# Performance work log

Hardware: AMD Instinct MI355X
Metric: run time of the kernel (lower is better)

The kernel has to match this reference:

```python
import jax, jax.numpy as jnp
import numpy as np

H = 128
B = 512
T = 1024
FUT = 64


def setup_inputs() -> dict:
    key = jax.random.key(0)
    ks = jax.random.split(key, 11)
    k = 1.0 / np.sqrt(H)  # torch LSTMCell/Linear init range
    u = lambda kk, shape: jax.random.uniform(kk, shape, jnp.float32, -k, k)
    return {
        "x": jax.random.normal(ks[0], (B, T), jnp.float32),
        "W_ih1": u(ks[1], (4 * H, 1)),
        "b_ih1": u(ks[2], (4 * H,)),
        "W_hh1": u(ks[3], (4 * H, H)),
        "b_hh1": u(ks[4], (4 * H,)),
        "W_ih2": u(ks[5], (4 * H, H)),
        "b_ih2": u(ks[6], (4 * H,)),
        "W_hh2": u(ks[7], (4 * H, H)),
        "b_hh2": u(ks[8], (4 * H,)),
        "W_out": u(ks[9], (1, H)),
        "b_out": u(ks[10], (1,)),
        "future": FUT,
    }


def _cell(x_t, h, c, W_ih, b_ih, W_hh, b_hh):
    # torch.nn.LSTMCell: gates ordered i, f, g, o
    g = x_t @ W_ih.T + h @ W_hh.T + (b_ih + b_hh)
    i, f, gg, o = jnp.split(g, 4, axis=-1)
    c_new = jax.nn.sigmoid(f) * c + jax.nn.sigmoid(i) * jnp.tanh(gg)
    h_new = jax.nn.sigmoid(o) * jnp.tanh(c_new)
    return h_new, c_new


def reference(x, W_ih1, b_ih1, W_hh1, b_hh1, W_ih2, b_ih2, W_hh2, b_hh2, W_out, b_out, future):
    Bn = x.shape[0]
    Hn = W_hh1.shape[1]
    z = jnp.zeros((Bn, Hn), x.dtype)

    def enc_step(carry, x_t):
        h1, c1, h2, c2 = carry
        h1, c1 = _cell(x_t, h1, c1, W_ih1, b_ih1, W_hh1, b_hh1)
        h2, c2 = _cell(h1, h2, c2, W_ih2, b_ih2, W_hh2, b_hh2)
        return (h1, c1, h2, c2), None

    xs = x.T[:, :, None]  # [T, B, 1]
    (h1, c1, h2, c2), _ = jax.lax.scan(enc_step, (z, z, z, z), xs)
    out0 = h2 @ W_out.T + b_out  # [B, 1]

    def fut_step(carry, _):
        h1, c1, h2, c2, out = carry
        h1, c1 = _cell(out, h1, c1, W_ih1, b_ih1, W_hh1, b_hh1)
        h2, c2 = _cell(h1, h2, c2, W_ih2, b_ih2, W_hh2, b_hh2)
        out = h2 @ W_out.T + b_out
        return (h1, c1, h2, c2, out), out

    _, fouts = jax.lax.scan(fut_step, (h1, c1, h2, c2, out0), None, length=future - 1)
    # torch cats [B,1] tensors on dim=1 -> [B, future]
    return jnp.concatenate([out0, fouts[:, :, 0].T], axis=1)
```

## Files before the change

### kernel.cpp

```cpp
#include <hip/hip_runtime.h>

#define HH 128
#define TT 1024
#define NFUT 64
#define MB 2
#define NBLK 256
#define NITER (TT + NFUT)

typedef _Float16 half8 __attribute__((ext_vector_type(8)));
typedef float floatx4 __attribute__((ext_vector_type(4)));

#define MFMA16(a, b, c) __builtin_amdgcn_mfma_f32_16x16x32_f16((a), (b), (c), 0, 0, 0)

__device__ __forceinline__ float sigm(float v) {
  return __builtin_amdgcn_rcpf(1.0f + __builtin_amdgcn_exp2f(v * -1.442695040888963f));
}
__device__ __forceinline__ float tanh_f(float v) {
  float a = __builtin_fabsf(v);
  float e = __builtin_amdgcn_exp2f(a * -2.885390081777927f);
  float r = (1.0f - e) * __builtin_amdgcn_rcpf(1.0f + e);
  return __builtin_copysignf(r, v);
}
__device__ __forceinline__ half8 ldw8(const float* __restrict__ p) {
  half8 r;
#pragma unroll
  for (int i = 0; i < 8; ++i) r[i] = (_Float16)p[i];
  return r;
}

__global__
__attribute__((amdgpu_flat_work_group_size(512, 512), amdgpu_waves_per_eu(2, 2)))
void lstm_kernel(
    const float* __restrict__ x,
    const float* __restrict__ W_ih1, const float* __restrict__ b_ih1,
    const float* __restrict__ W_hh1, const float* __restrict__ b_hh1,
    const float* __restrict__ W_ih2, const float* __restrict__ b_ih2,
    const float* __restrict__ W_hh2, const float* __restrict__ b_hh2,
    const float* __restrict__ W_out, const float* __restrict__ b_out,
    float* __restrict__ out)
{
  __shared__ __align__(16) _Float16 h1b[2][2048];
  __shared__ __align__(16) _Float16 h2b[2][2048];
  __shared__ float xs[TT * MB];
  __shared__ float opart[8 * MB];

  const int tid = (int)threadIdx.x;
  const int lane = tid & 63;
  const int w = tid >> 6;
  const int jl = lane & 15;
  const int rg = lane >> 4;
  const int j = w * 16 + jl;
  const int b0g = (int)blockIdx.x * MB;

  for (int idx = tid; idx < TT * MB; idx += 512) {
    int t = idx & (TT - 1);
    int bb = idx >> 10;
    xs[t * MB + bb] = x[(b0g + bb) * TT + t];
  }
  for (int idx = tid; idx < 2 * 2048; idx += 512) {
    h1b[idx >> 11][idx & 2047] = (_Float16)0.0f;
    h2b[idx >> 11][idx & 2047] = (_Float16)0.0f;
  }

  half8 A00, A01, A02, A03, A10, A11, A12, A13, A20, A21, A22, A23, A30, A31, A32, A33;
  half8 H00, H01, H02, H03, H10, H11, H12, H13, H20, H21, H22, H23, H30, H31, H32, H33;
  half8 I00, I01, I02, I03, I10, I11, I12, I13, I20, I21, I22, I23, I30, I31, I32, I33;
#define LDW(N, Q, P) do { \
    const float* _p = (P) + ((Q) * HH + j) * HH + rg * 8; \
    N##0 = ldw8(_p);      N##1 = ldw8(_p + 32); \
    N##2 = ldw8(_p + 64); N##3 = ldw8(_p + 96); } while (0)
  LDW(A0, 0, W_hh1); LDW(A1, 1, W_hh1); LDW(A2, 2, W_hh1); LDW(A3, 3, W_hh1);
  LDW(H0, 0, W_hh2); LDW(H1, 1, W_hh2); LDW(H2, 2, W_hh2); LDW(H3, 3, W_hh2);
  LDW(I0, 0, W_ih2); LDW(I1, 1, W_ih2); LDW(I2, 2, W_ih2); LDW(I3, 3, W_ih2);

  float bias1[4], bias2[4], wi1[4];
#pragma unroll
  for (int q = 0; q < 4; ++q) {
    bias1[q] = b_ih1[q * HH + j] + b_hh1[q * HH + j];
    bias2[q] = b_ih2[q * HH + j] + b_hh2[q * HH + j];
    wi1[q] = W_ih1[q * HH + j];
  }
  const float wo = W_out[j];
  const float bo = b_out[0];
  float c1a = 0.f, c1b = 0.f, c2a = 0.f, c2b = 0.f;

  __syncthreads();

  const int aoff = lane * 8;
  const int wb = ((j >> 5) << 9) + (((j >> 3) & 3) << 7) + (j & 7);

#define G2K(KF) do { \
    half8 bv = *(const half8*)(&h2b[prv][KF * 512 + aoff]); \
    g0 = MFMA16(bv, H0##KF, g0); g1 = MFMA16(bv, H1##KF, g1); \
    g2 = MFMA16(bv, H2##KF, g2); g3 = MFMA16(bv, H3##KF, g3); \
    half8 aw = *(const half8*)(&h1b[prv][KF * 512 + aoff]); \
    g0 = MFMA16(aw, I0##KF, g0); g1 = MFMA16(aw, I1##KF, g1); \
    g2 = MFMA16(aw, I2##KF, g2); g3 = MFMA16(aw, I3##KF, g3); } while (0)
#define G1K(KF) do { \
    half8 av = *(const half8*)(&h1b[prv][KF * 512 + aoff]); \
    a0 = MFMA16(av, A0##KF, a0); a1 = MFMA16(av, A1##KF, a1); \
    a2 = MFMA16(av, A2##KF, a2); a3 = MFMA16(av, A3##KF, a3); } while (0)

  for (int k = 0; k < NITER; ++k) {
    const int cur = k & 1;
    const int prv = cur ^ 1;

    floatx4 g0 = {0.f,0.f,0.f,0.f}, g1 = {0.f,0.f,0.f,0.f};
    floatx4 g2 = {0.f,0.f,0.f,0.f}, g3 = {0.f,0.f,0.f,0.f};
    __builtin_amdgcn_s_setprio(1);
    G2K(0); G2K(1); G2K(2); G2K(3);
    __builtin_amdgcn_s_setprio(0);

    if (k >= 1) {
      float gi0 = g0[0] + bias2[0], gi1 = g0[1] + bias2[0];
      float gf0 = g1[0] + bias2[1], gf1 = g1[1] + bias2[1];
      float gg0 = g2[0] + bias2[2], gg1 = g2[1] + bias2[2];
      float go0 = g3[0] + bias2[3], go1 = g3[1] + bias2[3];
      c2a = sigm(gf0) * c2a + sigm(gi0) * tanh_f(gg0);
      c2b = sigm(gf1) * c2b + sigm(gi1) * tanh_f(gg1);
      float h20 = sigm(go0) * tanh_f(c2a);
      float h21 = sigm(go1) * tanh_f(c2b);
      if (lane < 16) {
        h2b[cur][wb] = (_Float16)h20;
        h2b[cur][wb + 8] = (_Float16)h21;
      }
      if (k >= TT) {
        float p0 = h20 * wo, p1 = h21 * wo;
        p0 += __shfl_xor(p0, 1); p1 += __shfl_xor(p1, 1);
        p0 += __shfl_xor(p0, 2); p1 += __shfl_xor(p1, 2);
        p0 += __shfl_xor(p0, 4); p1 += __shfl_xor(p1, 4);
        p0 += __shfl_xor(p0, 8); p1 += __shfl_xor(p1, 8);
        if (lane == 0) {
          opart[w * MB + 0] = p0;
          opart[w * MB + 1] = p1;
        }
      }
    }

    floatx4 a0 = {0.f,0.f,0.f,0.f}, a1 = {0.f,0.f,0.f,0.f};
    floatx4 a2 = {0.f,0.f,0.f,0.f}, a3 = {0.f,0.f,0.f,0.f};
    __builtin_amdgcn_s_setprio(1);
    G1K(0); G1K(1); G1K(2); G1K(3);
    __builtin_amdgcn_s_setprio(0);

    float x0, x1;
    if (k < TT) {
      x0 = xs[k * MB + 0];
      x1 = xs[k * MB + 1];
    } else {
      __syncthreads();
      float s0 = bo, s1 = bo;
#pragma unroll
      for (int p = 0; p < 8; ++p) {
        s0 += opart[p * MB + 0];
        s1 += opart[p * MB + 1];
      }
      x0 = s0; x1 = s1;
      if (w == 0 && lane < MB) out[(b0g + lane) * NFUT + (k - TT)] = (lane == 0) ? s0 : s1;
    }

    if (k <= NITER - 2) {
      float gi0 = a0[0] + x0 * wi1[0] + bias1[0], gi1 = a0[1] + x1 * wi1[0] + bias1[0];
      float gf0 = a1[0] + x0 * wi1[1] + bias1[1], gf1 = a1[1] + x1 * wi1[1] + bias1[1];
      float gg0 = a2[0] + x0 * wi1[2] + bias1[2], gg1 = a2[1] + x1 * wi1[2] + bias1[2];
      float go0 = a3[0] + x0 * wi1[3] + bias1[3], go1 = a3[1] + x1 * wi1[3] + bias1[3];
      c1a = sigm(gf0) * c1a + sigm(gi0) * tanh_f(gg0);
      c1b = sigm(gf1) * c1b + sigm(gi1) * tanh_f(gg1);
      float h10 = sigm(go0) * tanh_f(c1a);
      float h11 = sigm(go1) * tanh_f(c1b);
      if (lane < 16) {
        h1b[cur][wb] = (_Float16)h10;
        h1b[cur][wb + 8] = (_Float16)h11;
      }
    }
    __syncthreads();
    __builtin_amdgcn_sched_barrier(0);
  }
}

extern "C" void kernel_launch(void* const* d_in, const int* in_sizes, int n_in,
                              void* d_out, int out_size, void* d_ws, size_t ws_size,
                              hipStream_t stream) {
  const float* x     = (const float*)d_in[0];
  const float* W_ih1 = (const float*)d_in[1];
  const float* b_ih1 = (const float*)d_in[2];
  const float* W_hh1 = (const float*)d_in[3];
  const float* b_hh1 = (const float*)d_in[4];
  const float* W_ih2 = (const float*)d_in[5];
  const float* b_ih2 = (const float*)d_in[6];
  const float* W_hh2 = (const float*)d_in[7];
  const float* b_hh2 = (const float*)d_in[8];
  const float* W_out = (const float*)d_in[9];
  const float* b_out = (const float*)d_in[10];
  (void)in_sizes; (void)n_in; (void)out_size; (void)d_ws; (void)ws_size;

  lstm_kernel<<<dim3(NBLK), dim3(512), 0, stream>>>(
      x, W_ih1, b_ih1, W_hh1, b_hh1, W_ih2, b_ih2, W_hh2, b_hh2, W_out, b_out,
      (float*)d_out);
}
```

Before: 1.582 ms.

## Halve block to 4 waves, each computing two 16-row hidden slices per gate

```diff
diff --git a/kernel.cpp b/kernel.cpp
--- a/kernel.cpp
+++ b/kernel.cpp
@@ -29,7 +29,7 @@
 }
 
 __global__
-__attribute__((amdgpu_flat_work_group_size(512, 512), amdgpu_waves_per_eu(2, 2)))
+__attribute__((amdgpu_flat_work_group_size(256, 256), amdgpu_waves_per_eu(1, 1)))
 void lstm_kernel(
     const float* __restrict__ x,
     const float* __restrict__ W_ih1, const float* __restrict__ b_ih1,
@@ -42,116 +42,148 @@
   __shared__ __align__(16) _Float16 h1b[2][2048];
   __shared__ __align__(16) _Float16 h2b[2][2048];
   __shared__ float xs[TT * MB];
-  __shared__ float opart[8 * MB];
+  __shared__ float opart[4 * MB];
 
   const int tid = (int)threadIdx.x;
   const int lane = tid & 63;
   const int w = tid >> 6;
   const int jl = lane & 15;
   const int rg = lane >> 4;
-  const int j = w * 16 + jl;
   const int b0g = (int)blockIdx.x * MB;
 
-  for (int idx = tid; idx < TT * MB; idx += 512) {
+  for (int idx = tid; idx < TT * MB; idx += 256) {
     int t = idx & (TT - 1);
     int bb = idx >> 10;
     xs[t * MB + bb] = x[(b0g + bb) * TT + t];
   }
-  for (int idx = tid; idx < 2 * 2048; idx += 512) {
+  for (int idx = tid; idx < 2 * 2048; idx += 256) {
     h1b[idx >> 11][idx & 2047] = (_Float16)0.0f;
     h2b[idx >> 11][idx & 2047] = (_Float16)0.0f;
   }
 
-  half8 A00, A01, A02, A03, A10, A11, A12, A13, A20, A21, A22, A23, A30, A31, A32, A33;
-  half8 H00, H01, H02, H03, H10, H11, H12, H13, H20, H21, H22, H23, H30, H31, H32, H33;
-  half8 I00, I01, I02, I03, I10, I11, I12, I13, I20, I21, I22, I23, I30, I31, I32, I33;
-#define LDW(N, Q, P) do { \
-    const float* _p = (P) + ((Q) * HH + j) * HH + rg * 8; \
-    N##0 = ldw8(_p);      N##1 = ldw8(_p + 32); \
-    N##2 = ldw8(_p + 64); N##3 = ldw8(_p + 96); } while (0)
-  LDW(A0, 0, W_hh1); LDW(A1, 1, W_hh1); LDW(A2, 2, W_hh1); LDW(A3, 3, W_hh1);
-  LDW(H0, 0, W_hh2); LDW(H1, 1, W_hh2); LDW(H2, 2, W_hh2); LDW(H3, 3, W_hh2);
-  LDW(I0, 0, W_ih2); LDW(I1, 1, W_ih2); LDW(I2, 2, W_ih2); LDW(I3, 3, W_ih2);
-
-  float bias1[4], bias2[4], wi1[4];
+  half8 A00,A01,A02,A03, A10,A11,A12,A13, A20,A21,A22,A23, A30,A31,A32,A33,
+        A40,A41,A42,A43, A50,A51,A52,A53, A60,A61,A62,A63, A70,A71,A72,A73;
+  half8 H00,H01,H02,H03, H10,H11,H12,H13, H20,H21,H22,H23, H30,H31,H32,H33,
+        H40,H41,H42,H43, H50,H51,H52,H53, H60,H61,H62,H63, H70,H71,H72,H73;
+  half8 I00,I01,I02,I03, I10,I11,I12,I13, I20,I21,I22,I23, I30,I31,I32,I33,
+        I40,I41,I42,I43, I50,I51,I52,I53, I60,I61,I62,I63, I70,I71,I72,I73;
+#define LDWS(N, S, Q, T, P) do { \
+    const float* _p = (P) + ((Q) * HH + (w * 32 + (T) * 16 + jl)) * HH + rg * 8; \
+    N##S##0 = ldw8(_p);      N##S##1 = ldw8(_p + 32); \
+    N##S##2 = ldw8(_p + 64); N##S##3 = ldw8(_p + 96); } while (0)
+  LDWS(A,0,0,0,W_hh1); LDWS(A,1,0,1,W_hh1); LDWS(A,2,1,0,W_hh1); LDWS(A,3,1,1,W_hh1);
+  LDWS(A,4,2,0,W_hh1); LDWS(A,5,2,1,W_hh1); LDWS(A,6,3,0,W_hh1); LDWS(A,7,3,1,W_hh1);
+  LDWS(H,0,0,0,W_hh2); LDWS(H,1,0,1,W_hh2); LDWS(H,2,1,0,W_hh2); LDWS(H,3,1,1,W_hh2);
+  LDWS(H,4,2,0,W_hh2); LDWS(H,5,2,1,W_hh2); LDWS(H,6,3,0,W_hh2); LDWS(H,7,3,1,W_hh2);
+  LDWS(I,0,0,0,W_ih2); LDWS(I,1,0,1,W_ih2); LDWS(I,2,1,0,W_ih2); LDWS(I,3,1,1,W_ih2);
+  LDWS(I,4,2,0,W_ih2); LDWS(I,5,2,1,W_ih2); LDWS(I,6,3,0,W_ih2); LDWS(I,7,3,1,W_ih2);
+
+  float b1[8], b2[8], w1[8];
 #pragma unroll
   for (int q = 0; q < 4; ++q) {
-    bias1[q] = b_ih1[q * HH + j] + b_hh1[q * HH + j];
-    bias2[q] = b_ih2[q * HH + j] + b_hh2[q * HH + j];
-    wi1[q] = W_ih1[q * HH + j];
-  }
-  const float wo = W_out[j];
+#pragma unroll
+    for (int t = 0; t < 2; ++t) {
+      int s = q * 2 + t;
+      int jt = w * 32 + t * 16 + jl;
+      b1[s] = b_ih1[q * HH + jt] + b_hh1[q * HH + jt];
+      b2[s] = b_ih2[q * HH + jt] + b_hh2[q * HH + jt];
+      w1[s] = W_ih1[q * HH + jt];
+    }
+  }
+  const float wo0 = W_out[w * 32 + jl];
+  const float wo1 = W_out[w * 32 + 16 + jl];
   const float bo = b_out[0];
-  float c1a = 0.f, c1b = 0.f, c2a = 0.f, c2b = 0.f;
+  float c1_00 = 0.f, c1_01 = 0.f, c1_10 = 0.f, c1_11 = 0.f;
+  float c2_00 = 0.f, c2_01 = 0.f, c2_10 = 0.f, c2_11 = 0.f;
 
   __syncthreads();
 
   const int aoff = lane * 8;
-  const int wb = ((j >> 5) << 9) + (((j >> 3) & 3) << 7) + (j & 7);
-
-#define G2K(KF) do { \
-    half8 bv = *(const half8*)(&h2b[prv][KF * 512 + aoff]); \
-    g0 = MFMA16(bv, H0##KF, g0); g1 = MFMA16(bv, H1##KF, g1); \
-    g2 = MFMA16(bv, H2##KF, g2); g3 = MFMA16(bv, H3##KF, g3); \
-    half8 aw = *(const half8*)(&h1b[prv][KF * 512 + aoff]); \
-    g0 = MFMA16(aw, I0##KF, g0); g1 = MFMA16(aw, I1##KF, g1); \
-    g2 = MFMA16(aw, I2##KF, g2); g3 = MFMA16(aw, I3##KF, g3); } while (0)
-#define G1K(KF) do { \
-    half8 av = *(const half8*)(&h1b[prv][KF * 512 + aoff]); \
-    a0 = MFMA16(av, A0##KF, a0); a1 = MFMA16(av, A1##KF, a1); \
-    a2 = MFMA16(av, A2##KF, a2); a3 = MFMA16(av, A3##KF, a3); } while (0)
+  const int j0 = w * 32 + jl, j1 = j0 + 16;
+  const int wb0 = ((j0 >> 5) << 9) + (((j0 >> 3) & 3) << 7) + (j0 & 7);
+  const int wb1 = ((j1 >> 5) << 9) + (((j1 >> 3) & 3) << 7) + (j1 & 7);
+
+#define C2K(K) do { \
+    half8 bv = *(const half8*)(&h2b[prv][K * 512 + aoff]); \
+    p0 = MFMA16(bv, H0##K, p0); p1 = MFMA16(bv, H1##K, p1); \
+    p2 = MFMA16(bv, H2##K, p2); p3 = MFMA16(bv, H3##K, p3); \
+    p4 = MFMA16(bv, H4##K, p4); p5 = MFMA16(bv, H5##K, p5); \
+    p6 = MFMA16(bv, H6##K, p6); p7 = MFMA16(bv, H7##K, p7); \
+    half8 aw = *(const half8*)(&h1b[prv][K * 512 + aoff]); \
+    p0 = MFMA16(aw, I0##K, p0); p1 = MFMA16(aw, I1##K, p1); \
+    p2 = MFMA16(aw, I2##K, p2); p3 = MFMA16(aw, I3##K, p3); \
+    p4 = MFMA16(aw, I4##K, p4); p5 = MFMA16(aw, I5##K, p5); \
+    p6 = MFMA16(aw, I6##K, p6); p7 = MFMA16(aw, I7##K, p7); } while (0)
+#define C1K(K) do { \
+    half8 av = *(const half8*)(&h1b[prv][K * 512 + aoff]); \
+    p0 = MFMA16(av, A0##K, p0); p1 = MFMA16(av, A1##K, p1); \
+    p2 = MFMA16(av, A2##K, p2); p3 = MFMA16(av, A3##K, p3); \
+    p4 = MFMA16(av, A4##K, p4); p5 = MFMA16(av, A5##K, p5); \
+    p6 = MFMA16(av, A6##K, p6); p7 = MFMA16(av, A7##K, p7); } while (0)
 
   for (int k = 0; k < NITER; ++k) {
     const int cur = k & 1;
     const int prv = cur ^ 1;
-
-    floatx4 g0 = {0.f,0.f,0.f,0.f}, g1 = {0.f,0.f,0.f,0.f};
-    floatx4 g2 = {0.f,0.f,0.f,0.f}, g3 = {0.f,0.f,0.f,0.f};
-    __builtin_amdgcn_s_setprio(1);
-    G2K(0); G2K(1); G2K(2); G2K(3);
-    __builtin_amdgcn_s_setprio(0);
+    const bool fut = (k >= TT);
+    const bool doC1 = (k <= NITER - 2);
+
+    floatx4 p0 = {0.f,0.f,0.f,0.f}, p1 = {0.f,0.f,0.f,0.f};
+    floatx4 p2 = {0.f,0.f,0.f,0.f}, p3 = {0.f,0.f,0.f,0.f};
+    floatx4 p4 = {0.f,0.f,0.f,0.f}, p5 = {0.f,0.f,0.f,0.f};
+    floatx4 p6 = {0.f,0.f,0.f,0.f}, p7 = {0.f,0.f,0.f,0.f};
+    C2K(0); C2K(1); C2K(2); C2K(3);
 
     if (k >= 1) {
-      float gi0 = g0[0] + bias2[0], gi1 = g0[1] + bias2[0];
-      float gf0 = g1[0] + bias2[1], gf1 = g1[1] + bias2[1];
-      float gg0 = g2[0] + bias2[2], gg1 = g2[1] + bias2[2];
-      float go0 = g3[0] + bias2[3], go1 = g3[1] + bias2[3];
-      c2a = sigm(gf0) * c2a + sigm(gi0) * tanh_f(gg0);
-      c2b = sigm(gf1) * c2b + sigm(gi1) * tanh_f(gg1);
-      float h20 = sigm(go0) * tanh_f(c2a);
-      float h21 = sigm(go1) * tanh_f(c2b);
+      float h2_00, h2_01, h2_10, h2_11;
+      {
+        float gi = p0[0] + b2[0], gf = p2[0] + b2[2], gg = p4[0] + b2[4], go = p6[0] + b2[6];
+        c2_00 = sigm(gf) * c2_00 + sigm(gi) * tanh_f(gg);
+        h2_00 = sigm(go) * tanh_f(c2_00);
+        gi = p0[1] + b2[0]; gf = p2[1] + b2[2]; gg = p4[1] + b2[4]; go = p6[1] + b2[6];
+        c2_01 = sigm(gf) * c2_01 + sigm(gi) * tanh_f(gg);
+        h2_01 = sigm(go) * tanh_f(c2_01);
+        gi = p1[0] + b2[1]; gf = p3[0] + b2[3]; gg = p5[0] + b2[5]; go = p7[0] + b2[7];
+        c2_10 = sigm(gf) * c2_10 + sigm(gi) * tanh_f(gg);
+        h2_10 = sigm(go) * tanh_f(c2_10);
+        gi = p1[1] + b2[1]; gf = p3[1] + b2[3]; gg = p5[1] + b2[5]; go = p7[1] + b2[7];
+        c2_11 = sigm(gf) * c2_11 + sigm(gi) * tanh_f(gg);
+        h2_11 = sigm(go) * tanh_f(c2_11);
+      }
       if (lane < 16) {
-        h2b[cur][wb] = (_Float16)h20;
-        h2b[cur][wb + 8] = (_Float16)h21;
-      }
-      if (k >= TT) {
-        float p0 = h20 * wo, p1 = h21 * wo;
-        p0 += __shfl_xor(p0, 1); p1 += __shfl_xor(p1, 1);
-        p0 += __shfl_xor(p0, 2); p1 += __shfl_xor(p1, 2);
-        p0 += __shfl_xor(p0, 4); p1 += __shfl_xor(p1, 4);
-        p0 += __shfl_xor(p0, 8); p1 += __shfl_xor(p1, 8);
+        h2b[cur][wb0] = (_Float16)h2_00;
+        h2b[cur][wb0 + 8] = (_Float16)h2_01;
+        h2b[cur][wb1] = (_Float16)h2_10;
+        h2b[cur][wb1 + 8] = (_Float16)h2_11;
+      }
+      if (fut) {
+        float u0 = h2_00 * wo0 + h2_10 * wo1;
+        float u1 = h2_01 * wo0 + h2_11 * wo1;
+        u0 += __shfl_xor(u0, 1); u1 += __shfl_xor(u1, 1);
+        u0 += __shfl_xor(u0, 2); u1 += __shfl_xor(u1, 2);
+        u0 += __shfl_xor(u0, 4); u1 += __shfl_xor(u1, 4);
+        u0 += __shfl_xor(u0, 8); u1 += __shfl_xor(u1, 8);
         if (lane == 0) {
-          opart[w * MB + 0] = p0;
-          opart[w * MB + 1] = p1;
+          opart[w * MB + 0] = u0;
+          opart[w * MB + 1] = u1;
         }
       }
     }
 
-    floatx4 a0 = {0.f,0.f,0.f,0.f}, a1 = {0.f,0.f,0.f,0.f};
-    floatx4 a2 = {0.f,0.f,0.f,0.f}, a3 = {0.f,0.f,0.f,0.f};
-    __builtin_amdgcn_s_setprio(1);
-    G1K(0); G1K(1); G1K(2); G1K(3);
-    __builtin_amdgcn_s_setprio(0);
+    p0 = (floatx4){0.f,0.f,0.f,0.f}; p1 = (floatx4){0.f,0.f,0.f,0.f};
+    p2 = (floatx4){0.f,0.f,0.f,0.f}; p3 = (floatx4){0.f,0.f,0.f,0.f};
+    p4 = (floatx4){0.f,0.f,0.f,0.f}; p5 = (floatx4){0.f,0.f,0.f,0.f};
+    p6 = (floatx4){0.f,0.f,0.f,0.f}; p7 = (floatx4){0.f,0.f,0.f,0.f};
+    C1K(0); C1K(1); C1K(2); C1K(3);
 
     float x0, x1;
-    if (k < TT) {
+    if (!fut) {
       x0 = xs[k * MB + 0];
       x1 = xs[k * MB + 1];
     } else {
       __syncthreads();
       float s0 = bo, s1 = bo;
 #pragma unroll
-      for (int p = 0; p < 8; ++p) {
+      for (int p = 0; p < 4; ++p) {
         s0 += opart[p * MB + 0];
         s1 += opart[p * MB + 1];
       }
@@ -159,22 +191,34 @@
       if (w == 0 && lane < MB) out[(b0g + lane) * NFUT + (k - TT)] = (lane == 0) ? s0 : s1;
     }
 
-    if (k <= NITER - 2) {
-      float gi0 = a0[0] + x0 * wi1[0] + bias1[0], gi1 = a0[1] + x1 * wi1[0] + bias1[0];
-      float gf0 = a1[0] + x0 * wi1[1] + bias1[1], gf1 = a1[1] + x1 * wi1[1] + bias1[1];
-      float gg0 = a2[0] + x0 * wi1[2] + bias1[2], gg1 = a2[1] + x1 * wi1[2] + bias1[2];
-      float go0 = a3[0] + x0 * wi1[3] + bias1[3], go1 = a3[1] + x1 * wi1[3] + bias1[3];
-      c1a = sigm(gf0) * c1a + sigm(gi0) * tanh_f(gg0);
-      c1b = sigm(gf1) * c1b + sigm(gi1) * tanh_f(gg1);
-      float h10 = sigm(go0) * tanh_f(c1a);
-      float h11 = sigm(go1) * tanh_f(c1b);
+    if (doC1) {
+      float h1_00, h1_01, h1_10, h1_11;
+      {
+        float gi = p0[0] + x0 * w1[0] + b1[0], gf = p2[0] + x0 * w1[2] + b1[2];
+        float gg = p4[0] + x0 * w1[4] + b1[4], go = p6[0] + x0 * w1[6] + b1[6];
+        c1_00 = sigm(gf) * c1_00 + sigm(gi) * tanh_f(gg);
+        h1_00 = sigm(go) * tanh_f(c1_00);
+        gi = p0[1] + x1 * w1[0] + b1[0]; gf = p2[1] + x1 * w1[2] + b1[2];
+        gg = p4[1] + x1 * w1[4] + b1[4]; go = p6[1] + x1 * w1[6] + b1[6];
+        c1_01 = sigm(gf) * c1_01 + sigm(gi) * tanh_f(gg);
+        h1_01 = sigm(go) * tanh_f(c1_01);
+        gi = p1[0] + x0 * w1[1] + b1[1]; gf = p3[0] + x0 * w1[3] + b1[3];
+        gg = p5[0] + x0 * w1[5] + b1[5]; go = p7[0] + x0 * w1[7] + b1[7];
+        c1_10 = sigm(gf) * c1_10 + sigm(gi) * tanh_f(gg);
+        h1_10 = sigm(go) * tanh_f(c1_10);
+        gi = p1[1] + x1 * w1[1] + b1[1]; gf = p3[1] + x1 * w1[3] + b1[3];
+        gg = p5[1] + x1 * w1[5] + b1[5]; go = p7[1] + x1 * w1[7] + b1[7];
+        c1_11 = sigm(gf) * c1_11 + sigm(gi) * tanh_f(gg);
+        h1_11 = sigm(go) * tanh_f(c1_11);
+      }
       if (lane < 16) {
-        h1b[cur][wb] = (_Float16)h10;
-        h1b[cur][wb + 8] = (_Float16)h11;
+        h1b[cur][wb0] = (_Float16)h1_00;
+        h1b[cur][wb0 + 8] = (_Float16)h1_01;
+        h1b[cur][wb1] = (_Float16)h1_10;
+        h1b[cur][wb1 + 8] = (_Float16)h1_11;
       }
     }
     __syncthreads();
-    __builtin_amdgcn_sched_barrier(0);
   }
 }
 
@@ -194,7 +238,7 @@
   const float* b_out = (const float*)d_in[10];
   (void)in_sizes; (void)n_in; (void)out_size; (void)d_ws; (void)ws_size;
 
-  lstm_kernel<<<dim3(NBLK), dim3(512), 0, stream>>>(
+  lstm_kernel<<<dim3(NBLK), dim3(256), 0, stream>>>(
       x, W_ih1, b_ih1, W_hh1, b_hh1, W_ih2, b_ih2, W_hh2, b_hh2, W_out, b_out,
       (float*)d_out);
 }
```

Result: slower. 2.528 ms (+59.8%).

## Split layer cells across wave halves with staggered two-phase schedule

Applied to the files above, without the earlier changes.

```diff
diff --git a/kernel.cpp b/kernel.cpp
--- a/kernel.cpp
+++ b/kernel.cpp
@@ -41,7 +41,7 @@
 {
   __shared__ __align__(16) _Float16 h1b[2][2048];
   __shared__ __align__(16) _Float16 h2b[2][2048];
-  __shared__ float xs[TT * MB];
+  __shared__ __align__(16) _Float16 xs[TT * MB];
   __shared__ float opart[8 * MB];
 
   const int tid = (int)threadIdx.x;
@@ -55,7 +55,7 @@
   for (int idx = tid; idx < TT * MB; idx += 512) {
     int t = idx & (TT - 1);
     int bb = idx >> 10;
-    xs[t * MB + bb] = x[(b0g + bb) * TT + t];
+    xs[t * MB + bb] = (_Float16)x[(b0g + bb) * TT + t];
   }
   for (int idx = tid; idx < 2 * 2048; idx += 512) {
     h1b[idx >> 11][idx & 2047] = (_Float16)0.0f;
@@ -89,89 +89,98 @@
   const int aoff = lane * 8;
   const int wb = ((j >> 5) << 9) + (((j >> 3) & 3) << 7) + (j & 7);
 
-#define G2K(KF) do { \
-    half8 bv = *(const half8*)(&h2b[prv][KF * 512 + aoff]); \
-    g0 = MFMA16(bv, H0##KF, g0); g1 = MFMA16(bv, H1##KF, g1); \
-    g2 = MFMA16(bv, H2##KF, g2); g3 = MFMA16(bv, H3##KF, g3); \
-    half8 aw = *(const half8*)(&h1b[prv][KF * 512 + aoff]); \
-    g0 = MFMA16(aw, I0##KF, g0); g1 = MFMA16(aw, I1##KF, g1); \
-    g2 = MFMA16(aw, I2##KF, g2); g3 = MFMA16(aw, I3##KF, g3); } while (0)
 #define G1K(KF) do { \
     half8 av = *(const half8*)(&h1b[prv][KF * 512 + aoff]); \
-    a0 = MFMA16(av, A0##KF, a0); a1 = MFMA16(av, A1##KF, a1); \
-    a2 = MFMA16(av, A2##KF, a2); a3 = MFMA16(av, A3##KF, a3); } while (0)
+    p0 = MFMA16(av, A0##KF, p0); p1 = MFMA16(av, A1##KF, p1); \
+    p2 = MFMA16(av, A2##KF, p2); p3 = MFMA16(av, A3##KF, p3); } while (0)
+#define G2K(KF) do { \
+    half8 av = *(const half8*)(&h2b[cur][KF * 512 + aoff]); \
+    p0 = MFMA16(av, H0##KF, p0); p1 = MFMA16(av, H1##KF, p1); \
+    p2 = MFMA16(av, H2##KF, p2); p3 = MFMA16(av, H3##KF, p3); \
+    half8 aw = *(const half8*)(&h1b[prv][KF * 512 + aoff]); \
+    p0 = MFMA16(aw, I0##KF, p0); p1 = MFMA16(aw, I1##KF, p1); \
+    p2 = MFMA16(aw, I2##KF, p2); p3 = MFMA16(aw, I3##KF, p3); } while (0)
+
+#define CELL1(X0, X1) do { \
+    floatx4 p0 = {0.f,0.f,0.f,0.f}, p1 = {0.f,0.f,0.f,0.f}; \
+    floatx4 p2 = {0.f,0.f,0.f,0.f}, p3 = {0.f,0.f,0.f,0.f}; \
+    __builtin_amdgcn_s_setprio(1); \
+    G1K(0); G1K(1); G1K(2); G1K(3); \
+    __builtin_amdgcn_s_setprio(0); \
+    float gi0 = p0[0] + (X0) * wi1[0] + bias1[0], gi1 = p0[1] + (X1) * wi1[0] + bias1[0]; \
+    float gf0 = p1[0] + (X0) * wi1[1] + bias1[1], gf1 = p1[1] + (X1) * wi1[1] + bias1[1]; \
+    float gg0 = p2[0] + (X0) * wi1[2] + bias1[2], gg1 = p2[1] + (X1) * wi1[2] + bias1[2]; \
+    float go0 = p3[0] + (X0) * wi1[3] + bias1[3], go1 = p3[1] + (X1) * wi1[3] + bias1[3]; \
+    c1a = sigm(gf0) * c1a + sigm(gi0) * tanh_f(gg0); \
+    c1b = sigm(gf1) * c1b + sigm(gi1) * tanh_f(gg1); \
+    float h10 = sigm(go0) * tanh_f(c1a); \
+    float h11 = sigm(go1) * tanh_f(c1b); \
+    if (lane < 16) { \
+      h1b[cur][wb] = (_Float16)h10; \
+      h1b[cur][wb + 8] = (_Float16)h11; \
+    } } while (0)
+
+#define CELL2(DOPROJ) do { \
+    floatx4 p0 = {0.f,0.f,0.f,0.f}, p1 = {0.f,0.f,0.f,0.f}; \
+    floatx4 p2 = {0.f,0.f,0.f,0.f}, p3 = {0.f,0.f,0.f,0.f}; \
+    __builtin_amdgcn_s_setprio(1); \
+    G2K(0); G2K(1); G2K(2); G2K(3); \
+    __builtin_amdgcn_s_setprio(0); \
+    float gi0 = p0[0] + bias2[0], gi1 = p0[1] + bias2[0]; \
+    float gf0 = p1[0] + bias2[1], gf1 = p1[1] + bias2[1]; \
+    float gg0 = p2[0] + bias2[2], gg1 = p2[1] + bias2[2]; \
+    float go0 = p3[0] + bias2[3], go1 = p3[1] + bias2[3]; \
+    c2a = sigm(gf0) * c2a + sigm(gi0) * tanh_f(gg0); \
+    c2b = sigm(gf1) * c2b + sigm(gi1) * tanh_f(gg1); \
+    float h20 = sigm(go0) * tanh_f(c2a); \
+    float h21 = sigm(go1) * tanh_f(c2b); \
+    if (lane < 16) { \
+      h2b[prv][wb] = (_Float16)h20; \
+      h2b[prv][wb + 8] = (_Float16)h21; \
+    } \
+    if (DOPROJ) { \
+      float q0 = h20 * wo, q1 = h21 * wo; \
+      q0 += __shfl_xor(q0, 1); q1 += __shfl_xor(q1, 1); \
+      q0 += __shfl_xor(q0, 2); q1 += __shfl_xor(q1, 2); \
+      q0 += __shfl_xor(q0, 4); q1 += __shfl_xor(q1, 4); \
+      q0 += __shfl_xor(q0, 8); q1 += __shfl_xor(q1, 8); \
+      if (lane == 0) { \
+        opart[w * MB + 0] = q0; \
+        opart[w * MB + 1] = q1; \
+      } \
+    } } while (0)
 
   for (int k = 0; k < NITER; ++k) {
     const int cur = k & 1;
     const int prv = cur ^ 1;
 
-    floatx4 g0 = {0.f,0.f,0.f,0.f}, g1 = {0.f,0.f,0.f,0.f};
-    floatx4 g2 = {0.f,0.f,0.f,0.f}, g3 = {0.f,0.f,0.f,0.f};
-    __builtin_amdgcn_s_setprio(1);
-    G2K(0); G2K(1); G2K(2); G2K(3);
-    __builtin_amdgcn_s_setprio(0);
-
-    if (k >= 1) {
-      float gi0 = g0[0] + bias2[0], gi1 = g0[1] + bias2[0];
-      float gf0 = g1[0] + bias2[1], gf1 = g1[1] + bias2[1];
-      float gg0 = g2[0] + bias2[2], gg1 = g2[1] + bias2[2];
-      float go0 = g3[0] + bias2[3], go1 = g3[1] + bias2[3];
-      c2a = sigm(gf0) * c2a + sigm(gi0) * tanh_f(gg0);
-      c2b = sigm(gf1) * c2b + sigm(gi1) * tanh_f(gg1);
-      float h20 = sigm(go0) * tanh_f(c2a);
-      float h21 = sigm(go1) * tanh_f(c2b);
-      if (lane < 16) {
-        h2b[cur][wb] = (_Float16)h20;
-        h2b[cur][wb + 8] = (_Float16)h21;
+    if (k < TT) {
+      const float ex0 = (float)xs[k * MB + 0];
+      const float ex1 = (float)xs[k * MB + 1];
+      if (w < 4) {
+        CELL1(ex0, ex1);
+      } else if (k >= 1) {
+        CELL2(false);
       }
-      if (k >= TT) {
-        float p0 = h20 * wo, p1 = h21 * wo;
-        p0 += __shfl_xor(p0, 1); p1 += __shfl_xor(p1, 1);
-        p0 += __shfl_xor(p0, 2); p1 += __shfl_xor(p1, 2);
-        p0 += __shfl_xor(p0, 4); p1 += __shfl_xor(p1, 4);
-        p0 += __shfl_xor(p0, 8); p1 += __shfl_xor(p1, 8);
-        if (lane == 0) {
-          opart[w * MB + 0] = p0;
-          opart[w * MB + 1] = p1;
-        }
+      __syncthreads();
+      __builtin_amdgcn_sched_barrier(0);
+      if (w < 4) {
+        if (k >= 1) CELL2(false);
+      } else {
+        CELL1(ex0, ex1);
       }
-    }
-
-    floatx4 a0 = {0.f,0.f,0.f,0.f}, a1 = {0.f,0.f,0.f,0.f};
-    floatx4 a2 = {0.f,0.f,0.f,0.f}, a3 = {0.f,0.f,0.f,0.f};
-    __builtin_amdgcn_s_setprio(1);
-    G1K(0); G1K(1); G1K(2); G1K(3);
-    __builtin_amdgcn_s_setprio(0);
-
-    float x0, x1;
-    if (k < TT) {
-      x0 = xs[k * MB + 0];
-      x1 = xs[k * MB + 1];
     } else {
+      CELL2(true);
       __syncthreads();
+      __builtin_amdgcn_sched_barrier(0);
       float s0 = bo, s1 = bo;
 #pragma unroll
       for (int p = 0; p < 8; ++p) {
         s0 += opart[p * MB + 0];
         s1 += opart[p * MB + 1];
       }
-      x0 = s0; x1 = s1;
       if (w == 0 && lane < MB) out[(b0g + lane) * NFUT + (k - TT)] = (lane == 0) ? s0 : s1;
-    }
-
-    if (k <= NITER - 2) {
-      float gi0 = a0[0] + x0 * wi1[0] + bias1[0], gi1 = a0[1] + x1 * wi1[0] + bias1[0];
-      float gf0 = a1[0] + x0 * wi1[1] + bias1[1], gf1 = a1[1] + x1 * wi1[1] + bias1[1];
-      float gg0 = a2[0] + x0 * wi1[2] + bias1[2], gg1 = a2[1] + x1 * wi1[2] + bias1[2];
-      float go0 = a3[0] + x0 * wi1[3] + bias1[3], go1 = a3[1] + x1 * wi1[3] + bias1[3];
-      c1a = sigm(gf0) * c1a + sigm(gi0) * tanh_f(gg0);
-      c1b = sigm(gf1) * c1b + sigm(gi1) * tanh_f(gg1);
-      float h10 = sigm(go0) * tanh_f(c1a);
-      float h11 = sigm(go1) * tanh_f(c1b);
-      if (lane < 16) {
-        h1b[cur][wb] = (_Float16)h10;
-        h1b[cur][wb + 8] = (_Float16)h11;
-      }
+      if (k <= NITER - 2) CELL1(s0, s1);
     }
     __syncthreads();
     __builtin_amdgcn_sched_barrier(0);
```

New measurement: 1.636 ms. 3.4% more time.
